# Kernel optimization log

Measured on AMD Instinct MI355X. Metric: run time of the kernel, lower is better.

The kernel has to match this reference:

```python
import jax, jax.numpy as jnp
import numpy as np

KSIZE, H, W = 11, 256, 256
IN_C, OUT_C, B = 3, 64, 4


def _foveated_coords(height, width, k):
    """Integer foveated sampling coords [H, W, k, k] for y and x.

    Ring scale per kernel tap: Chebyshev dist from center -> 1/3/5/7.
    Matches FoveatedSamplingConv2d._create_all_foveated_kernels, where
    coords are exact integers, so bilinear grid_sample == integer gather.
    """
    c = k // 2
    ki = np.arange(k)
    dist = np.maximum(np.abs(ki[:, None] - c), np.abs(ki[None, :] - c))  # [k,k]
    scale = np.where(dist <= 1, 1, np.where(dist == 2, 3, np.where(dist == 3, 5, 7)))
    off_y = (ki[:, None] - c) * scale  # [k,k]
    off_x = (ki[None, :] - c) * scale  # [k,k]
    yy = np.arange(height)[:, None, None, None]
    xx = np.arange(width)[None, :, None, None]
    sy = np.clip(yy + off_y[None, None], 0, height - 1)  # [H,W,k,k]
    sx = np.clip(xx + off_x[None, None], 0, width - 1)   # [H,W,k,k]
    return jnp.asarray(sy, jnp.int32), jnp.asarray(sx, jnp.int32)


def setup_inputs() -> dict:
    key = jax.random.key(0)
    k1, k2, k3 = jax.random.split(key, 3)
    x = jax.random.normal(k1, (B, IN_C, H, W), dtype=jnp.float32)
    # Kaiming-uniform-ish init scale (exact distribution irrelevant for correctness)
    fan_in = IN_C * KSIZE * KSIZE
    bound = 1.0 / np.sqrt(fan_in)
    weight = jax.random.uniform(k2, (OUT_C, IN_C, KSIZE, KSIZE), dtype=jnp.float32,
                                minval=-bound, maxval=bound)
    bias = jax.random.uniform(k3, (OUT_C,), dtype=jnp.float32, minval=-bound, maxval=bound)
    sy, sx = _foveated_coords(H, W, KSIZE)
    return {"x": x, "weight": weight, "bias": bias, "sy": sy, "sx": sx}


def reference(x, weight, bias, sy, sx):
    # Irregular gather: sampled[b,c,h,w,ki,kj] = x[b,c, sy[h,w,ki,kj], sx[h,w,ki,kj]]
    sampled = x[:, :, sy, sx]  # [B, C, H, W, k, k]
    out = jnp.einsum('bchwkl,ockl->bohw', sampled, weight)
    return out + bias[None, :, None, None]
```

## Files before the change

kernel.cpp:

```cpp
#include <hip/hip_runtime.h>


#define HH 256
#define WW 256
#define INC 3
#define OC 64
#define KS 11
#define BB 4
#define KPC 128
#define NKC 12
#define PH 326
#define PW 512
#define PAD 35
#define NPAR 4
#define HALFR 163

typedef __attribute__((ext_vector_type(4))) float f32x4;
typedef __attribute__((ext_vector_type(8))) short s16x8;
typedef unsigned int u32;
typedef unsigned short u16;

static __device__ __forceinline__ u16 f2bf(float f) {
    u32 u = __builtin_bit_cast(u32, f);
    u32 r = (u + 0x7FFFu + ((u >> 16) & 1u)) >> 16;
    return (u16)r;
}

__global__ void __launch_bounds__(256)
prep_fused(const float* __restrict__ x, const float* __restrict__ w,
           u16* __restrict__ xs, u16* __restrict__ wf) {
    const int tid = threadIdx.x;
    if (blockIdx.x < 96) {
        int i = blockIdx.x * 256 + tid;
        int j    = i & 7;
        int lane = (i >> 3) & 63;
        int ot   = (i >> 9) & 3;
        int kc   = i >> 11;
        int o  = ot * 16 + (lane & 15);
        int k  = kc * 32 + ((lane >> 4) << 3) + j;
        int c  = k >> 7;
        int tt = k & 127;
        float val = 0.f;
        if (tt < 121) {
            int ky = tt / 11, kx = tt % 11;
            val = w[((o * INC + c) * KS + ky) * KS + kx];
        }
        wf[i] = f2bf(val);
    } else {
        const int pb = blockIdx.x - 96;
        const int k  = pb & 7;
        const int i  = pb >> 3;
        const int r  = i * 2 + (tid >> 7);
        const int zl = r / HALFR;
        const int pz = r - zl * HALFR;
        const int b    = k >> 1;
        const int py   = (k & 1) * HALFR + pz;
        const int c    = zl % INC;
        const int par  = zl / INC;
        const int z    = (b * NPAR + par) * INC + c;
        const int px0  = (tid & 127) * 4;
        const int sy   = min(max(py - PAD, 0), HH - 1);
        const float* src = x + (((size_t)b * INC + c) * HH + sy) * WW;
        ushort4 o4;
        int s0 = min(max(px0 + 0 - PAD + par, 0), WW - 1);
        int s1 = min(max(px0 + 1 - PAD + par, 0), WW - 1);
        int s2 = min(max(px0 + 2 - PAD + par, 0), WW - 1);
        int s3 = min(max(px0 + 3 - PAD + par, 0), WW - 1);
        o4.x = f2bf(src[s0]); o4.y = f2bf(src[s1]);
        o4.z = f2bf(src[s2]); o4.w = f2bf(src[s3]);
        *(ushort4*)&xs[((size_t)z * PH + py) * PW + px0] = o4;
    }
}

__global__ void __launch_bounds__(256, 3)
fov_mfma5(const u16* __restrict__ xs, const u16* __restrict__ wf,
          const float* __restrict__ bias, float* __restrict__ out) {
    __shared__ u32 offF[NKC * 32];
    const int tid = threadIdx.x;
    for (int t = tid; t < NKC * 32; t += 256) {
        int c = t >> 7, tt = t & 127;
        int dy = 0, dx = 0;
        if (tt < 121) {
            int ky = tt / 11, kx = tt - (tt / 11) * 11;
            int ay = ky - 5, ax = kx - 5;
            int d = max(abs(ay), abs(ax));
            int sc = (d <= 1) ? 1 : (d == 2 ? 3 : (d == 3 ? 5 : 7));
            dy = ay * sc; dx = ax * sc;
        }
        int par = (PAD + dx) & 3;
        offF[t] = (u32)(((((par * INC + c) * PH) + (PAD + dy)) * PW
                         + (PAD + dx - par)) * 2);
    }
    __syncthreads();

    const int lane = tid & 63;
    const int wv   = tid >> 6;
    const int obid = (blockIdx.x & 7) * 128 + (blockIdx.x >> 3);
    const int b = obid >> 8;
    const int h = obid & 255;
    const int g16 = lane & 15;
    const int kg  = lane >> 4;

    const char* xpb = (const char*)(xs + (size_t)b * (NPAR * INC * PH * PW));
    const u32 pxoff = (u32)((h * PW + wv * 64 + 4 * g16) * 2);
    const s16x8* wbase = (const s16x8*)wf;

    f32x4 acc[4][4];
#pragma unroll
    for (int T = 0; T < 4; ++T)
#pragma unroll
        for (int ob = 0; ob < 4; ++ob) acc[T][ob] = (f32x4){0, 0, 0, 0};

    uint2 G[2][8];
    s16x8 A[2][4];

    {
        const uint4* fp = (const uint4*)&offF[kg * 8];
        const uint4 fA = fp[0], fB = fp[1];
        G[0][0] = *(const uint2*)(xpb + (pxoff + fA.x));
        G[0][1] = *(const uint2*)(xpb + (pxoff + fA.y));
        G[0][2] = *(const uint2*)(xpb + (pxoff + fA.z));
        G[0][3] = *(const uint2*)(xpb + (pxoff + fA.w));
        G[0][4] = *(const uint2*)(xpb + (pxoff + fB.x));
        G[0][5] = *(const uint2*)(xpb + (pxoff + fB.y));
        G[0][6] = *(const uint2*)(xpb + (pxoff + fB.z));
        G[0][7] = *(const uint2*)(xpb + (pxoff + fB.w));
        const s16x8* wp = wbase + lane;
        A[0][0] = wp[0]; A[0][1] = wp[64]; A[0][2] = wp[128]; A[0][3] = wp[192];
    }

#pragma unroll
    for (int kc = 0; kc < NKC; ++kc) {
        const int cur = kc & 1;
        const int nxt = cur ^ 1;
        if (kc + 1 < NKC) {
            const uint4* fp = (const uint4*)&offF[(kc + 1) * 32 + kg * 8];
            const uint4 fA = fp[0], fB = fp[1];
            G[nxt][0] = *(const uint2*)(xpb + (pxoff + fA.x));
            G[nxt][1] = *(const uint2*)(xpb + (pxoff + fA.y));
            G[nxt][2] = *(const uint2*)(xpb + (pxoff + fA.z));
            G[nxt][3] = *(const uint2*)(xpb + (pxoff + fA.w));
            G[nxt][4] = *(const uint2*)(xpb + (pxoff + fB.x));
            G[nxt][5] = *(const uint2*)(xpb + (pxoff + fB.y));
            G[nxt][6] = *(const uint2*)(xpb + (pxoff + fB.z));
            G[nxt][7] = *(const uint2*)(xpb + (pxoff + fB.w));
            const s16x8* wp = wbase + (((kc + 1) << 8) + lane);
            A[nxt][0] = wp[0];   A[nxt][1] = wp[64];
            A[nxt][2] = wp[128]; A[nxt][3] = wp[192];
        }
        __builtin_amdgcn_s_setprio(1);
#pragma unroll
        for (int T = 0; T < 4; ++T) {
            const u32 sel = (T & 1) ? 0x07060302u : 0x05040100u;
            const bool hi = (T >> 1) != 0;
            union { u32 u[4]; s16x8 v; } bu;
            bu.u[0] = __builtin_amdgcn_perm(hi ? G[cur][1].y : G[cur][1].x,
                                            hi ? G[cur][0].y : G[cur][0].x, sel);
            bu.u[1] = __builtin_amdgcn_perm(hi ? G[cur][3].y : G[cur][3].x,
                                            hi ? G[cur][2].y : G[cur][2].x, sel);
            bu.u[2] = __builtin_amdgcn_perm(hi ? G[cur][5].y : G[cur][5].x,
                                            hi ? G[cur][4].y : G[cur][4].x, sel);
            bu.u[3] = __builtin_amdgcn_perm(hi ? G[cur][7].y : G[cur][7].x,
                                            hi ? G[cur][6].y : G[cur][6].x, sel);

            acc[T][0] = __builtin_amdgcn_mfma_f32_16x16x32_bf16(A[cur][0], bu.v, acc[T][0], 0, 0, 0);
            acc[T][1] = __builtin_amdgcn_mfma_f32_16x16x32_bf16(A[cur][1], bu.v, acc[T][1], 0, 0, 0);
            acc[T][2] = __builtin_amdgcn_mfma_f32_16x16x32_bf16(A[cur][2], bu.v, acc[T][2], 0, 0, 0);
            acc[T][3] = __builtin_amdgcn_mfma_f32_16x16x32_bf16(A[cur][3], bu.v, acc[T][3], 0, 0, 0);
        }
        __builtin_amdgcn_s_setprio(0);
    }

    const int orow = kg << 2;
    const float4* bp = (const float4*)bias;
#pragma unroll
    for (int ob = 0; ob < 4; ++ob) {
        const float4 bb = bp[ob * 4 + kg];
        const float bv[4] = {bb.x, bb.y, bb.z, bb.w};
#pragma unroll
        for (int r = 0; r < 4; ++r) {
            const int o = ob * 16 + orow + r;
            f32x4 st;
            st[0] = acc[0][ob][r] + bv[r];
            st[1] = acc[1][ob][r] + bv[r];
            st[2] = acc[2][ob][r] + bv[r];
            st[3] = acc[3][ob][r] + bv[r];
            float* op = out + (((size_t)b * OC + o) * HH + h) * WW + wv * 64 + 4 * g16;
            __builtin_nontemporal_store(st, (f32x4*)op);
        }
    }
}

__global__ void fovconv_transpose_w(const float* __restrict__ w,
                                    float* __restrict__ wT) {
    int i = blockIdx.x * 256 + threadIdx.x;
    const int N = OC * INC * KS * KS;
    if (i < N) {
        int o  = i / (INC * KS * KS);
        int ct = i % (INC * KS * KS);
        wT[ct * OC + o] = w[i];
    }
}

__global__ void __launch_bounds__(256)
fovconv_main(const float* __restrict__ x, const float* __restrict__ wT,
             const float* __restrict__ bias, float* __restrict__ out) {
    const int wpix = threadIdx.x;
    const int h    = blockIdx.x & (HH - 1);
    const int b    = blockIdx.x >> 8;
    float acc[OC];
#pragma unroll
    for (int o = 0; o < OC; ++o) acc[o] = 0.f;
    const float* xbp = x + (size_t)b * INC * HH * WW;
    for (int k = 0; k < KS; ++k) {
        const int dy = k - 5;
        for (int l = 0; l < KS; ++l) {
            const int dx = l - 5;
            const int d  = max(abs(dy), abs(dx));
            const int scale = (d <= 1) ? 1 : (d == 2 ? 3 : (d == 3 ? 5 : 7));
            const int sy = min(max(h + dy * scale, 0), HH - 1);
            const int sx = min(max(wpix + dx * scale, 0), WW - 1);
            const int base = sy * WW + sx;
            const int t = k * KS + l;
#pragma unroll
            for (int c = 0; c < INC; ++c) {
                const float xv = xbp[c * (HH * WW) + base];
                const float* wp = wT + (c * (KS * KS) + t) * OC;
#pragma unroll
                for (int o = 0; o < OC; ++o)
                    acc[o] = fmaf(xv, wp[o], acc[o]);
            }
        }
    }
    float* op = out + (((size_t)b * OC) * HH + h) * WW + wpix;
#pragma unroll
    for (int o = 0; o < OC; ++o)
        op[(size_t)o * HH * WW] = acc[o] + bias[o];
}

extern "C" void kernel_launch(void* const* d_in, const int* in_sizes, int n_in,
                              void* d_out, int out_size, void* d_ws, size_t ws_size,
                              hipStream_t stream) {
    const float* x    = (const float*)d_in[0];
    const float* wgt  = (const float*)d_in[1];
    const float* bias = (const float*)d_in[2];
    float* out = (float*)d_out;

    const size_t xs_bytes = (size_t)BB * NPAR * INC * PH * PW * 2;
    const size_t wf_bytes = (size_t)NKC * 4 * 64 * 8 * 2;

    if (ws_size >= xs_bytes + wf_bytes) {
        u16* xsb = (u16*)d_ws;
        u16* wf  = (u16*)((char*)d_ws + xs_bytes);
        prep_fused<<<96 + 978 * 8, 256, 0, stream>>>(x, wgt, xsb, wf);
        fov_mfma5<<<BB * HH, 256, 0, stream>>>(xsb, wf, bias, out);
    } else {
        float* wT = (float*)d_ws;
        const int NW = OC * INC * KS * KS;
        fovconv_transpose_w<<<(NW + 255) / 256, 256, 0, stream>>>(wgt, wT);
        fovconv_main<<<BB * HH, 256, 0, stream>>>(x, wT, bias, out);
    }
}
```

Baseline: 36.65 us.

## Stage distinct tap rows into LDS via global_load_lds instead of 4-parity padded copies

The prep kernel now writes a single padded bf16 copy of the input rather than four parity-shifted copies, so the workspace and the prep launch shrink about fourfold. The main kernel loads the 69 distinct source rows (23 unique dy offsets times 3 channels) for its output row into shared memory with global_load_lds. It then gathers unaligned 4-element windows from LDS using three dword reads and alignbit, instead of per-tap 8-byte global gathers. This removes redundant global and L2 traffic but adds about 45KB of LDS per block, which may limit occupancy, and more LDS reads plus ALU work for the unaligned extraction.

Measured after the change: 38.24 us. +4.4%, slower.

```diff
diff --git a/kernel.cpp b/kernel.cpp
--- a/kernel.cpp
+++ b/kernel.cpp
@@ -7,18 +7,23 @@
 #define OC 64
 #define KS 11
 #define BB 4
-#define KPC 128
 #define NKC 12
 #define PH 326
 #define PW 512
 #define PAD 35
-#define NPAR 4
-#define HALFR 163
+#define NDY 23
+#define NROW 69
+#define ROWB 672
+#define ROWU16 336
 
 typedef __attribute__((ext_vector_type(4))) float f32x4;
 typedef __attribute__((ext_vector_type(8))) short s16x8;
 typedef unsigned int u32;
 typedef unsigned short u16;
+
+static __device__ const int dyv[NDY] = {
+    -35, -28, -21, -15, -14, -10, -7, -6, -5, -3, -1,
+      0,   1,   3,   5,   6,   7, 10, 14, 15, 21, 28, 35};
 
 static __device__ __forceinline__ u16 f2bf(float f) {
     u32 u = __builtin_bit_cast(u32, f);
@@ -51,58 +56,74 @@
         const int k  = pb & 7;
         const int i  = pb >> 3;
         const int r  = i * 2 + (tid >> 7);
-        const int zl = r / HALFR;
-        const int pz = r - zl * HALFR;
-        const int b    = k >> 1;
-        const int py   = (k & 1) * HALFR + pz;
-        const int c    = zl % INC;
-        const int par  = zl / INC;
-        const int z    = (b * NPAR + par) * INC + c;
-        const int px0  = (tid & 127) * 4;
-        const int sy   = min(max(py - PAD, 0), HH - 1);
-        const float* src = x + (((size_t)b * INC + c) * HH + sy) * WW;
-        ushort4 o4;
-        int s0 = min(max(px0 + 0 - PAD + par, 0), WW - 1);
-        int s1 = min(max(px0 + 1 - PAD + par, 0), WW - 1);
-        int s2 = min(max(px0 + 2 - PAD + par, 0), WW - 1);
-        int s3 = min(max(px0 + 3 - PAD + par, 0), WW - 1);
-        o4.x = f2bf(src[s0]); o4.y = f2bf(src[s1]);
-        o4.z = f2bf(src[s2]); o4.w = f2bf(src[s3]);
-        *(ushort4*)&xs[((size_t)z * PH + py) * PW + px0] = o4;
+        if (r < 3 * 163) {
+            const int c   = r / 163;
+            const int pz  = r - c * 163;
+            const int py  = (k & 1) * 163 + pz;
+            const int b   = k >> 1;
+            const int px0 = (tid & 127) * 4;
+            const int sy  = min(max(py - PAD, 0), HH - 1);
+            const float* src = x + (((size_t)b * INC + c) * HH + sy) * WW;
+            ushort4 o4;
+            int s0 = min(max(px0 + 0 - PAD, 0), WW - 1);
+            int s1 = min(max(px0 + 1 - PAD, 0), WW - 1);
+            int s2 = min(max(px0 + 2 - PAD, 0), WW - 1);
+            int s3 = min(max(px0 + 3 - PAD, 0), WW - 1);
+            o4.x = f2bf(src[s0]); o4.y = f2bf(src[s1]);
+            o4.z = f2bf(src[s2]); o4.w = f2bf(src[s3]);
+            *(ushort4*)&xs[(((size_t)b * INC + c) * PH + py) * PW + px0] = o4;
+        }
     }
 }
 
 __global__ void __launch_bounds__(256, 3)
-fov_mfma5(const u16* __restrict__ xs, const u16* __restrict__ wf,
-          const float* __restrict__ bias, float* __restrict__ out) {
-    __shared__ u32 offF[NKC * 32];
-    const int tid = threadIdx.x;
+fov_lds(const u16* __restrict__ xs, const u16* __restrict__ wf,
+        const float* __restrict__ bias, float* __restrict__ out) {
+    __shared__ __align__(16) u16 sdata[NROW * ROWU16];
+    __shared__ u32 offL[NKC * 32];
+
+    const int tid  = threadIdx.x;
+    const int lane = tid & 63;
+    const int wv   = tid >> 6;
+    const int obid = (blockIdx.x & 7) * 128 + (blockIdx.x >> 3);
+    const int b = obid >> 8;
+    const int h = obid & 255;
+
     for (int t = tid; t < NKC * 32; t += 256) {
         int c = t >> 7, tt = t & 127;
-        int dy = 0, dx = 0;
+        u32 v = 0;
         if (tt < 121) {
             int ky = tt / 11, kx = tt - (tt / 11) * 11;
             int ay = ky - 5, ax = kx - 5;
             int d = max(abs(ay), abs(ax));
             int sc = (d <= 1) ? 1 : (d == 2 ? 3 : (d == 3 ? 5 : 7));
-            dy = ay * sc; dx = ax * sc;
-        }
-        int par = (PAD + dx) & 3;
-        offF[t] = (u32)(((((par * INC + c) * PH) + (PAD + dy)) * PW
-                         + (PAD + dx - par)) * 2);
+            int dy = ay * sc, dx = ax * sc;
+            int di = 0;
+#pragma unroll
+            for (int s = 0; s < NDY; ++s) if (dyv[s] == dy) di = s;
+            v = (u32)((c * NDY + di) * ROWB + (PAD + dx) * 2);
+        }
+        offL[t] = v;
+    }
+
+    for (int ri = wv; ri < NROW; ri += 4) {
+        int c  = (ri >= 2 * NDY) ? 2 : (ri >= NDY ? 1 : 0);
+        int di = ri - c * NDY;
+        int py = h + PAD + dyv[di];
+        const char* src = (const char*)(xs + (((size_t)b * INC + c) * PH + py) * PW);
+        if (lane < ROWB / 16) {
+            __builtin_amdgcn_global_load_lds(
+                (const __attribute__((address_space(1))) void*)(src + lane * 16),
+                (__attribute__((address_space(3))) void*)&sdata[ri * ROWU16],
+                16, 0, 0);
+        }
     }
     __syncthreads();
 
-    const int lane = tid & 63;
-    const int wv   = tid >> 6;
-    const int obid = (blockIdx.x & 7) * 128 + (blockIdx.x >> 3);
-    const int b = obid >> 8;
-    const int h = obid & 255;
     const int g16 = lane & 15;
     const int kg  = lane >> 4;
-
-    const char* xpb = (const char*)(xs + (size_t)b * (NPAR * INC * PH * PW));
-    const u32 pxoff = (u32)((h * PW + wv * 64 + 4 * g16) * 2);
+    const u32 lane_base = (u32)((wv * 64 + 4 * g16) * 2);
+    const u32* s32 = (const u32*)sdata;
     const s16x8* wbase = (const s16x8*)wf;
 
     f32x4 acc[4][4];
@@ -111,20 +132,8 @@
 #pragma unroll
         for (int ob = 0; ob < 4; ++ob) acc[T][ob] = (f32x4){0, 0, 0, 0};
 
-    uint2 G[2][8];
     s16x8 A[2][4];
-
     {
-        const uint4* fp = (const uint4*)&offF[kg * 8];
-        const uint4 fA = fp[0], fB = fp[1];
-        G[0][0] = *(const uint2*)(xpb + (pxoff + fA.x));
-        G[0][1] = *(const uint2*)(xpb + (pxoff + fA.y));
-        G[0][2] = *(const uint2*)(xpb + (pxoff + fA.z));
-        G[0][3] = *(const uint2*)(xpb + (pxoff + fA.w));
-        G[0][4] = *(const uint2*)(xpb + (pxoff + fB.x));
-        G[0][5] = *(const uint2*)(xpb + (pxoff + fB.y));
-        G[0][6] = *(const uint2*)(xpb + (pxoff + fB.z));
-        G[0][7] = *(const uint2*)(xpb + (pxoff + fB.w));
         const s16x8* wp = wbase + lane;
         A[0][0] = wp[0]; A[0][1] = wp[64]; A[0][2] = wp[128]; A[0][3] = wp[192];
     }
@@ -134,34 +143,33 @@
         const int cur = kc & 1;
         const int nxt = cur ^ 1;
         if (kc + 1 < NKC) {
-            const uint4* fp = (const uint4*)&offF[(kc + 1) * 32 + kg * 8];
-            const uint4 fA = fp[0], fB = fp[1];
-            G[nxt][0] = *(const uint2*)(xpb + (pxoff + fA.x));
-            G[nxt][1] = *(const uint2*)(xpb + (pxoff + fA.y));
-            G[nxt][2] = *(const uint2*)(xpb + (pxoff + fA.z));
-            G[nxt][3] = *(const uint2*)(xpb + (pxoff + fA.w));
-            G[nxt][4] = *(const uint2*)(xpb + (pxoff + fB.x));
-            G[nxt][5] = *(const uint2*)(xpb + (pxoff + fB.y));
-            G[nxt][6] = *(const uint2*)(xpb + (pxoff + fB.z));
-            G[nxt][7] = *(const uint2*)(xpb + (pxoff + fB.w));
             const s16x8* wp = wbase + (((kc + 1) << 8) + lane);
             A[nxt][0] = wp[0];   A[nxt][1] = wp[64];
             A[nxt][2] = wp[128]; A[nxt][3] = wp[192];
         }
+        const uint4* lp = (const uint4*)&offL[kc * 32 + kg * 8];
+        const uint4 oA = lp[0], oB = lp[1];
+        const u32 offs[8] = {oA.x, oA.y, oA.z, oA.w, oB.x, oB.y, oB.z, oB.w};
+        u32 lo[8], hi[8];
+#pragma unroll
+        for (int j = 0; j < 8; ++j) {
+            u32 addr = lane_base + offs[j];
+            u32 i0 = addr >> 2;
+            u32 sh = (addr & 2) << 3;
+            u32 w0 = s32[i0], w1 = s32[i0 + 1], w2 = s32[i0 + 2];
+            lo[j] = __builtin_amdgcn_alignbit(w1, w0, sh);
+            hi[j] = __builtin_amdgcn_alignbit(w2, w1, sh);
+        }
         __builtin_amdgcn_s_setprio(1);
 #pragma unroll
         for (int T = 0; T < 4; ++T) {
             const u32 sel = (T & 1) ? 0x07060302u : 0x05040100u;
-            const bool hi = (T >> 1) != 0;
+            const bool up = (T >> 1) != 0;
             union { u32 u[4]; s16x8 v; } bu;
-            bu.u[0] = __builtin_amdgcn_perm(hi ? G[cur][1].y : G[cur][1].x,
-                                            hi ? G[cur][0].y : G[cur][0].x, sel);
-            bu.u[1] = __builtin_amdgcn_perm(hi ? G[cur][3].y : G[cur][3].x,
-                                            hi ? G[cur][2].y : G[cur][2].x, sel);
-            bu.u[2] = __builtin_amdgcn_perm(hi ? G[cur][5].y : G[cur][5].x,
-                                            hi ? G[cur][4].y : G[cur][4].x, sel);
-            bu.u[3] = __builtin_amdgcn_perm(hi ? G[cur][7].y : G[cur][7].x,
-                                            hi ? G[cur][6].y : G[cur][6].x, sel);
+            bu.u[0] = __builtin_amdgcn_perm(up ? hi[1] : lo[1], up ? hi[0] : lo[0], sel);
+            bu.u[1] = __builtin_amdgcn_perm(up ? hi[3] : lo[3], up ? hi[2] : lo[2], sel);
+            bu.u[2] = __builtin_amdgcn_perm(up ? hi[5] : lo[5], up ? hi[4] : lo[4], sel);
+            bu.u[3] = __builtin_amdgcn_perm(up ? hi[7] : lo[7], up ? hi[6] : lo[6], sel);
 
             acc[T][0] = __builtin_amdgcn_mfma_f32_16x16x32_bf16(A[cur][0], bu.v, acc[T][0], 0, 0, 0);
             acc[T][1] = __builtin_amdgcn_mfma_f32_16x16x32_bf16(A[cur][1], bu.v, acc[T][1], 0, 0, 0);
@@ -246,14 +254,14 @@
     const float* bias = (const float*)d_in[2];
     float* out = (float*)d_out;
 
-    const size_t xs_bytes = (size_t)BB * NPAR * INC * PH * PW * 2;
+    const size_t xs_bytes = (size_t)BB * INC * PH * PW * 2;
     const size_t wf_bytes = (size_t)NKC * 4 * 64 * 8 * 2;
 
     if (ws_size >= xs_bytes + wf_bytes) {
         u16* xsb = (u16*)d_ws;
         u16* wf  = (u16*)((char*)d_ws + xs_bytes);
-        prep_fused<<<96 + 978 * 8, 256, 0, stream>>>(x, wgt, xsb, wf);
-        fov_mfma5<<<BB * HH, 256, 0, stream>>>(xsb, wf, bias, out);
+        prep_fused<<<96 + 245 * 8, 256, 0, stream>>>(x, wgt, xsb, wf);
+        fov_lds<<<BB * HH, 256, 0, stream>>>(xsb, wf, bias, out);
     } else {
         float* wT = (float*)d_ws;
         const int NW = OC * INC * KS * KS;
```

## Triple-buffer gather loads two chunks ahead and raise occupancy bound to four

Applied to the files above, without the earlier changes.

The input gather registers go from double to triple buffering, so each K-chunk's gathered pixels are issued two iterations before use, while weights stay double-buffered. This gives gather latency more MFMA work to hide behind. The launch bounds hint rises from 3 to 4 waves per SIMD, which caps registers per thread lower even though the deeper pipeline needs more registers. That combination may cause spills or force the compiler to serialize the prefetches.

Result: slower. 135.7 us (+270.2%).

```diff
diff --git a/kernel.cpp b/kernel.cpp
--- a/kernel.cpp
+++ b/kernel.cpp
@@ -7,7 +7,6 @@
 #define OC 64
 #define KS 11
 #define BB 4
-#define KPC 128
 #define NKC 12
 #define PH 326
 #define PW 512
@@ -72,7 +71,7 @@
     }
 }
 
-__global__ void __launch_bounds__(256, 3)
+__global__ void __launch_bounds__(256, 4)
 fov_mfma5(const u16* __restrict__ xs, const u16* __restrict__ wf,
           const float* __restrict__ bias, float* __restrict__ out) {
     __shared__ u32 offF[NKC * 32];
@@ -111,42 +110,39 @@
 #pragma unroll
         for (int ob = 0; ob < 4; ++ob) acc[T][ob] = (f32x4){0, 0, 0, 0};
 
-    uint2 G[2][8];
+    uint2 G[3][8];
     s16x8 A[2][4];
 
+#define STAGE_G(S, KC)                                                    \
+    {                                                                     \
+        const uint4* fp = (const uint4*)&offF[(KC) * 32 + kg * 8];        \
+        const uint4 fA = fp[0], fB = fp[1];                               \
+        G[S][0] = *(const uint2*)(xpb + (pxoff + fA.x));                  \
+        G[S][1] = *(const uint2*)(xpb + (pxoff + fA.y));                  \
+        G[S][2] = *(const uint2*)(xpb + (pxoff + fA.z));                  \
+        G[S][3] = *(const uint2*)(xpb + (pxoff + fA.w));                  \
+        G[S][4] = *(const uint2*)(xpb + (pxoff + fB.x));                  \
+        G[S][5] = *(const uint2*)(xpb + (pxoff + fB.y));                  \
+        G[S][6] = *(const uint2*)(xpb + (pxoff + fB.z));                  \
+        G[S][7] = *(const uint2*)(xpb + (pxoff + fB.w));                  \
+    }
+
+    STAGE_G(0, 0)
+    STAGE_G(1, 1)
     {
-        const uint4* fp = (const uint4*)&offF[kg * 8];
-        const uint4 fA = fp[0], fB = fp[1];
-        G[0][0] = *(const uint2*)(xpb + (pxoff + fA.x));
-        G[0][1] = *(const uint2*)(xpb + (pxoff + fA.y));
-        G[0][2] = *(const uint2*)(xpb + (pxoff + fA.z));
-        G[0][3] = *(const uint2*)(xpb + (pxoff + fA.w));
-        G[0][4] = *(const uint2*)(xpb + (pxoff + fB.x));
-        G[0][5] = *(const uint2*)(xpb + (pxoff + fB.y));
-        G[0][6] = *(const uint2*)(xpb + (pxoff + fB.z));
-        G[0][7] = *(const uint2*)(xpb + (pxoff + fB.w));
         const s16x8* wp = wbase + lane;
         A[0][0] = wp[0]; A[0][1] = wp[64]; A[0][2] = wp[128]; A[0][3] = wp[192];
     }
 
 #pragma unroll
     for (int kc = 0; kc < NKC; ++kc) {
-        const int cur = kc & 1;
-        const int nxt = cur ^ 1;
+        const int cur = kc % 3;
+        const int pre = (kc + 2) % 3;
+        if (kc + 2 < NKC) STAGE_G(pre, kc + 2)
         if (kc + 1 < NKC) {
-            const uint4* fp = (const uint4*)&offF[(kc + 1) * 32 + kg * 8];
-            const uint4 fA = fp[0], fB = fp[1];
-            G[nxt][0] = *(const uint2*)(xpb + (pxoff + fA.x));
-            G[nxt][1] = *(const uint2*)(xpb + (pxoff + fA.y));
-            G[nxt][2] = *(const uint2*)(xpb + (pxoff + fA.z));
-            G[nxt][3] = *(const uint2*)(xpb + (pxoff + fA.w));
-            G[nxt][4] = *(const uint2*)(xpb + (pxoff + fB.x));
-            G[nxt][5] = *(const uint2*)(xpb + (pxoff + fB.y));
-            G[nxt][6] = *(const uint2*)(xpb + (pxoff + fB.z));
-            G[nxt][7] = *(const uint2*)(xpb + (pxoff + fB.w));
             const s16x8* wp = wbase + (((kc + 1) << 8) + lane);
-            A[nxt][0] = wp[0];   A[nxt][1] = wp[64];
-            A[nxt][2] = wp[128]; A[nxt][3] = wp[192];
+            A[(kc + 1) & 1][0] = wp[0];   A[(kc + 1) & 1][1] = wp[64];
+            A[(kc + 1) & 1][2] = wp[128]; A[(kc + 1) & 1][3] = wp[192];
         }
         __builtin_amdgcn_s_setprio(1);
 #pragma unroll
@@ -163,13 +159,14 @@
             bu.u[3] = __builtin_amdgcn_perm(hi ? G[cur][7].y : G[cur][7].x,
                                             hi ? G[cur][6].y : G[cur][6].x, sel);
 
-            acc[T][0] = __builtin_amdgcn_mfma_f32_16x16x32_bf16(A[cur][0], bu.v, acc[T][0], 0, 0, 0);
-            acc[T][1] = __builtin_amdgcn_mfma_f32_16x16x32_bf16(A[cur][1], bu.v, acc[T][1], 0, 0, 0);
-            acc[T][2] = __builtin_amdgcn_mfma_f32_16x16x32_bf16(A[cur][2], bu.v, acc[T][2], 0, 0, 0);
-            acc[T][3] = __builtin_amdgcn_mfma_f32_16x16x32_bf16(A[cur][3], bu.v, acc[T][3], 0, 0, 0);
+            acc[T][0] = __builtin_amdgcn_mfma_f32_16x16x32_bf16(A[kc & 1][0], bu.v, acc[T][0], 0, 0, 0);
+            acc[T][1] = __builtin_amdgcn_mfma_f32_16x16x32_bf16(A[kc & 1][1], bu.v, acc[T][1], 0, 0, 0);
+            acc[T][2] = __builtin_amdgcn_mfma_f32_16x16x32_bf16(A[kc & 1][2], bu.v, acc[T][2], 0, 0, 0);
+            acc[T][3] = __builtin_amdgcn_mfma_f32_16x16x32_bf16(A[kc & 1][3], bu.v, acc[T][3], 0, 0, 0);
         }
         __builtin_amdgcn_s_setprio(0);
     }
+#undef STAGE_G
 
     const int orow = kg << 2;
     const float4* bp = (const float4*)bias;
```
